# Kernel optimization log

Hardware: AMD Instinct MI355X
Metric: run time of the kernel (lower is better)

## Reference

```python
import jax, jax.numpy as jnp
import numpy as np

B, N = 16, 512          # graphs, nodes per graph (equal-size dynamic batch)
IN, HID, OUT, K = 256, 128, 256, 16  # hidden = in_dim // red_factor
EPS = 1e-5


def setup_inputs() -> dict:
    key = jax.random.key(0)
    ks = jax.random.split(key, 12)
    def lin(k, fi, fo):
        return jax.random.normal(k, (fi, fo), jnp.float32) / np.sqrt(fi).astype(np.float32)
    return {
        "obj_encs": jax.random.normal(ks[0], (B * N, IN), jnp.float32),
        "n_nodes": jnp.full((B,), N, dtype=jnp.int32),
        # self-graph-attention params (in -> hidden), with residual projection
        "Wq": lin(ks[1], IN, HID), "bq": jnp.zeros((HID,), jnp.float32),
        "Wk": lin(ks[2], IN, HID), "bk": jnp.zeros((HID,), jnp.float32),
        "Wv": lin(ks[3], IN, HID), "bv": jnp.zeros((HID,), jnp.float32),
        "Wr": lin(ks[4], IN, HID), "br": jnp.zeros((HID,), jnp.float32),
        # EdgeConv (local+global => 2*HID input features)
        "Wc": lin(ks[5], 2 * HID, OUT), "bc": jnp.zeros((OUT,), jnp.float32),
        # LayerNorm affine
        "ln_scale": jnp.ones((OUT,), jnp.float32),
        "ln_bias": jnp.zeros((OUT,), jnp.float32),
    }


def _forward(obj_encs, n_nodes, Wq, bq, Wk, bk, Wv, bv, Wr, br, Wc, bc, ln_scale, ln_bias):
    # dynamic batching: equal-size graphs per n_nodes -> reshape [B, N, IN]
    x = obj_encs.reshape(B, N, IN)

    # --- SelfGraphAttentionLinear (per-graph dot-product attention, residual) ---
    q = x @ Wq + bq                      # [B, N, HID]
    kk = x @ Wk + bk
    v = x @ Wv + bv
    attn = jax.nn.softmax(jnp.einsum('bnd,bmd->bnm', q, kk) / np.sqrt(HID).astype(np.float32), axis=-1)
    h = jnp.einsum('bnm,bmd->bnd', attn, v) + (x @ Wr + br)  # residual projection

    # --- GraphConv: kNN (euclidean) within each graph ---
    sq = jnp.sum(h * h, axis=-1)                             # [B, N]
    dist = sq[:, :, None] + sq[:, None, :] - 2.0 * jnp.einsum('bnd,bmd->bnm', h, h)
    _, idx = jax.lax.top_k(-dist, K)                         # [B, N, K] (self included)

    nb = jax.vmap(lambda hb, ib: hb[ib])(h, idx)             # [B, N, K, HID]
    hc = h[:, :, None, :]                                    # [B, N, 1, HID]
    # features='local+global': [x_i, x_j - x_i]
    e = jnp.concatenate([jnp.broadcast_to(hc, nb.shape), nb - hc], axis=-1)  # [B,N,K,2H]

    y = jnp.einsum('bnkf,fo->bnko', e, Wc) + bc              # [B, N, K, OUT]
    y = jnp.max(y, axis=2)                                   # reduction='max' over k

    mu = jnp.mean(y, axis=-1, keepdims=True)
    var = jnp.mean((y - mu) ** 2, axis=-1, keepdims=True)
    y = (y - mu) / jnp.sqrt(var + EPS) * ln_scale + ln_bias  # LayerNorm
    return jax.nn.selu(y).reshape(B * N, OUT)


def reference(obj_encs, n_nodes, Wq, bq, Wk, bk, Wv, bv, Wr, br, Wc, bc, ln_scale, ln_bias):
    return _forward(obj_encs, n_nodes, Wq, bq, Wk, bk, Wv, bv, Wr, br, Wc, bc, ln_scale, ln_bias)
```

## Files before the change

kernel.cpp:

```cpp
#include <hip/hip_runtime.h>
#include <math.h>

#define NB   16
#define NN   512
#define FIN  256
#define HID  128
#define FOUT 256
#define TOPK 16
#define ROWS (NB*NN)
#define LN_EPS 1e-5f

#define BK  32
#define LDK 40

typedef __attribute__((ext_vector_type(8))) short  bf16x8;
typedef __attribute__((ext_vector_type(4))) float  f32x4;

__device__ __forceinline__ ushort f2bf_rn(float x) {
    uint u = __float_as_uint(x);
    u += 0x7fff + ((u >> 16) & 1);
    return (ushort)(u >> 16);
}
__device__ __forceinline__ float bf2f(ushort h) {
    return __uint_as_float(((uint)h) << 16);
}
__device__ __forceinline__ void split2(float x, ushort& hi, ushort& lo) {
    hi = f2bf_rn(x);
    lo = f2bf_rn(x - bf2f(hi));
}

__device__ __forceinline__ void stage_rows64(ushort (*Dh)[LDK], ushort (*Dl)[LDK],
                                             const float* __restrict__ src,
                                             int rstride, int tid)
{
    const int r = tid >> 2, seg = (tid & 3) * 8;
    const float* p = src + (size_t)r * rstride + seg;
    #pragma unroll
    for (int i = 0; i < 2; i++) {
        const float4 q = *(const float4*)(p + 4*i);
        ushort h0,l0,h1,l1,h2,l2,h3,l3;
        split2(q.x,h0,l0); split2(q.y,h1,l1);
        split2(q.z,h2,l2); split2(q.w,h3,l3);
        *(ushort4*)&Dh[r][seg + 4*i] = make_ushort4(h0,h1,h2,h3);
        *(ushort4*)&Dl[r][seg + 4*i] = make_ushort4(l0,l1,l2,l3);
    }
}

__device__ __forceinline__ void stage_cols64(ushort (*Dh)[LDK], ushort (*Dl)[LDK],
                                             const float* __restrict__ src,
                                             int ldn, int tid)
{
    const int n = tid & 63, kh = (tid >> 6) * 8;
    const float* p = src + (size_t)kh * ldn + n;
    ushort hh[8], ll[8];
    #pragma unroll
    for (int i = 0; i < 8; i++) split2(p[(size_t)i * ldn], hh[i], ll[i]);
    *(ushort4*)&Dh[n][kh]     = make_ushort4(hh[0],hh[1],hh[2],hh[3]);
    *(ushort4*)&Dh[n][kh + 4] = make_ushort4(hh[4],hh[5],hh[6],hh[7]);
    *(ushort4*)&Dl[n][kh]     = make_ushort4(ll[0],ll[1],ll[2],ll[3]);
    *(ushort4*)&Dl[n][kh + 4] = make_ushort4(ll[4],ll[5],ll[6],ll[7]);
}

__device__ __forceinline__ void mma_step64(const ushort (*Ah)[LDK], const ushort (*Al)[LDK],
                                           const ushort (*Bh)[LDK], const ushort (*Bl)[LDK],
                                           f32x4 acc[2][2], int wr, int wc, int lane)
{
    const int q8 = (lane >> 4) * 8, m = lane & 15;
    bf16x8 ah[2], al[2], bh[2], bl[2];
    #pragma unroll
    for (int i = 0; i < 2; i++) {
        ah[i] = *(const bf16x8*)&Ah[wr + 16*i + m][q8];
        al[i] = *(const bf16x8*)&Al[wr + 16*i + m][q8];
        bh[i] = *(const bf16x8*)&Bh[wc + 16*i + m][q8];
        bl[i] = *(const bf16x8*)&Bl[wc + 16*i + m][q8];
    }
    #pragma unroll
    for (int i = 0; i < 2; i++)
        #pragma unroll
        for (int j = 0; j < 2; j++) {
            acc[i][j] = __builtin_amdgcn_mfma_f32_16x16x32_bf16(ah[i], bh[j], acc[i][j], 0, 0, 0);
            acc[i][j] = __builtin_amdgcn_mfma_f32_16x16x32_bf16(ah[i], bl[j], acc[i][j], 0, 0, 0);
            acc[i][j] = __builtin_amdgcn_mfma_f32_16x16x32_bf16(al[i], bh[j], acc[i][j], 0, 0, 0);
        }
}

#define MM64_PROLOGUE()                                                     \
    __shared__ ushort Ah[64][LDK], Al[64][LDK], Bh[64][LDK], Bl[64][LDK];   \
    const int tid = threadIdx.x, lane = tid & 63, wv = tid >> 6;            \
    const int wr = (wv >> 1) * 32, wc = (wv & 1) * 32;                      \
    f32x4 acc[2][2];                                                        \
    _Pragma("unroll")                                                       \
    for (int i = 0; i < 2; i++)                                             \
        _Pragma("unroll")                                                   \
        for (int j = 0; j < 2; j++)                                         \
            acc[i][j] = (f32x4){0.f, 0.f, 0.f, 0.f};

__global__ __launch_bounds__(256) void k_proj_m(
    const float* __restrict__ X,
    const float* __restrict__ Wq, const float* __restrict__ bq,
    const float* __restrict__ Wk, const float* __restrict__ bk,
    const float* __restrict__ Wv, const float* __restrict__ bv,
    const float* __restrict__ Wr, const float* __restrict__ br,
    float* __restrict__ Y)
{
    const int widx = blockIdx.x >> 1;
    const int ch   = (blockIdx.x & 1) * 64;
    const int br0  = blockIdx.y * 64;
    const float* W; const float* bias;
    if      (widx == 0) { W = Wq; bias = bq; }
    else if (widx == 1) { W = Wk; bias = bk; }
    else if (widx == 2) { W = Wv; bias = bv; }
    else                { W = Wr; bias = br; }

    MM64_PROLOGUE();

    for (int k0 = 0; k0 < FIN; k0 += BK) {
        stage_rows64(Ah, Al, X + (size_t)br0 * FIN + k0, FIN, tid);
        stage_cols64(Bh, Bl, W + (size_t)k0 * HID + ch, HID, tid);
        __syncthreads();
        mma_step64(Ah, Al, Bh, Bl, acc, wr, wc, lane);
        __syncthreads();
    }

    const int m = lane & 15, q4 = (lane >> 4) * 4;
    #pragma unroll
    for (int i = 0; i < 2; i++)
        #pragma unroll
        for (int reg = 0; reg < 4; reg++) {
            const int grow = br0 + wr + 16*i + q4 + reg;
            #pragma unroll
            for (int j = 0; j < 2; j++) {
                const int c = ch + wc + 16*j + m;
                Y[(size_t)grow * 512 + widx * 128 + c] = acc[i][j][reg] + bias[c];
            }
        }
}

__global__ __launch_bounds__(256) void k_scores_m(
    const float* __restrict__ Y, float* __restrict__ S)
{
    const int b = blockIdx.z;
    const int m0 = blockIdx.x * 64, n0 = blockIdx.y * 64;
    const float scale = 0.08838834764831845f;
    const float* Yb = Y + (size_t)b * NN * 512;

    MM64_PROLOGUE();

    for (int k0 = 0; k0 < HID; k0 += BK) {
        stage_rows64(Ah, Al, Yb + (size_t)n0 * 512 + k0,       512, tid);
        stage_rows64(Bh, Bl, Yb + (size_t)m0 * 512 + 128 + k0, 512, tid);
        __syncthreads();
        mma_step64(Ah, Al, Bh, Bl, acc, wr, wc, lane);
        __syncthreads();
    }

    float* Sb = S + (size_t)b * NN * NN;
    const int m = lane & 15, q4 = (lane >> 4) * 4;
    #pragma unroll
    for (int i = 0; i < 2; i++)
        #pragma unroll
        for (int reg = 0; reg < 4; reg++) {
            const int n = n0 + wr + 16*i + q4 + reg;
            #pragma unroll
            for (int j = 0; j < 2; j++)
                Sb[(size_t)n * NN + m0 + wc + 16*j + m] = acc[i][j][reg] * scale;
        }
}

__global__ __launch_bounds__(256) void k_softmax(float* __restrict__ S)
{
    float* p = S + (size_t)blockIdx.x * NN;
    const int tid = threadIdx.x;
    const int lane = tid & 63, wave = tid >> 6;
    __shared__ float red[4];

    float v0 = p[tid], v1 = p[tid + 256];
    float mx = fmaxf(v0, v1);
    #pragma unroll
    for (int off = 32; off > 0; off >>= 1) mx = fmaxf(mx, __shfl_down(mx, off));
    if (lane == 0) red[wave] = mx;
    __syncthreads();
    mx = fmaxf(fmaxf(red[0], red[1]), fmaxf(red[2], red[3]));
    __syncthreads();

    float e0 = __expf(v0 - mx), e1 = __expf(v1 - mx);
    float s = e0 + e1;
    #pragma unroll
    for (int off = 32; off > 0; off >>= 1) s += __shfl_down(s, off);
    if (lane == 0) red[wave] = s;
    __syncthreads();
    s = red[0] + red[1] + red[2] + red[3];
    const float inv = 1.0f / s;
    p[tid] = e0 * inv;
    p[tid + 256] = e1 * inv;
}

__global__ __launch_bounds__(256) void k_hgemm_m(
    const float* __restrict__ S, const float* __restrict__ Y,
    float* __restrict__ H)
{
    const int c0 = blockIdx.x * 64;
    const int n0 = blockIdx.y * 64;
    const int b  = blockIdx.z;
    const float* P = S + (size_t)b * NN * NN;

    MM64_PROLOGUE();

    for (int k0 = 0; k0 < NN; k0 += BK) {
        stage_rows64(Ah, Al, P + (size_t)n0 * NN + k0, NN, tid);
        stage_cols64(Bh, Bl, Y + ((size_t)(b * NN + k0)) * 512 + 256 + c0, 512, tid);
        __syncthreads();
        mma_step64(Ah, Al, Bh, Bl, acc, wr, wc, lane);
        __syncthreads();
    }

    const int m = lane & 15, q4 = (lane >> 4) * 4;
    #pragma unroll
    for (int i = 0; i < 2; i++)
        #pragma unroll
        for (int reg = 0; reg < 4; reg++) {
            const int gr = b * NN + n0 + wr + 16*i + q4 + reg;
            #pragma unroll
            for (int j = 0; j < 2; j++) {
                const int c = c0 + wc + 16*j + m;
                H[(size_t)gr * HID + c] = acc[i][j][reg] + Y[(size_t)gr * 512 + 384 + c];
            }
        }
}

__global__ __launch_bounds__(256) void k_sq(
    const float* __restrict__ H, float* __restrict__ SQ)
{
    const int row = blockIdx.x * 4 + (threadIdx.x >> 6);
    const int lane = threadIdx.x & 63;
    float a = H[(size_t)row*HID + lane];
    float c = H[(size_t)row*HID + 64 + lane];
    float s = a*a + c*c;
    #pragma unroll
    for (int off = 32; off > 0; off >>= 1) s += __shfl_down(s, off);
    if (lane == 0) SQ[row] = s;
}

__global__ __launch_bounds__(256) void k_ab_m(
    const float* __restrict__ H, const float* __restrict__ Wc,
    const float* __restrict__ bc, float* __restrict__ AB)
{
    const int ct  = blockIdx.x;
    const int br0 = blockIdx.y * 64;
    const bool bhalf = ct >= 4;
    const int c0 = (ct & 3) * 64;

    MM64_PROLOGUE();

    for (int k0 = 0; k0 < HID; k0 += BK) {
        stage_rows64(Ah, Al, H + (size_t)br0 * HID + k0, HID, tid);
        {
            const int n = tid & 63, kh = (tid >> 6) * 8;
            ushort hh[8], ll[8];
            #pragma unroll
            for (int i = 0; i < 8; i++) {
                const int k = k0 + kh + i;
                const float wbot = Wc[(size_t)(HID + k) * FOUT + c0 + n];
                const float val = bhalf ? wbot
                                        : (Wc[(size_t)k * FOUT + c0 + n] - wbot);
                split2(val, hh[i], ll[i]);
            }
            *(ushort4*)&Bh[n][kh]     = make_ushort4(hh[0],hh[1],hh[2],hh[3]);
            *(ushort4*)&Bh[n][kh + 4] = make_ushort4(hh[4],hh[5],hh[6],hh[7]);
            *(ushort4*)&Bl[n][kh]     = make_ushort4(ll[0],ll[1],ll[2],ll[3]);
            *(ushort4*)&Bl[n][kh + 4] = make_ushort4(ll[4],ll[5],ll[6],ll[7]);
        }
        __syncthreads();
        mma_step64(Ah, Al, Bh, Bl, acc, wr, wc, lane);
        __syncthreads();
    }

    const int m = lane & 15, q4 = (lane >> 4) * 4;
    #pragma unroll
    for (int i = 0; i < 2; i++)
        #pragma unroll
        for (int reg = 0; reg < 4; reg++) {
            const int grow = br0 + wr + 16*i + q4 + reg;
            #pragma unroll
            for (int j = 0; j < 2; j++) {
                const int c = wc + 16*j + m;
                const float add = bhalf ? 0.0f : bc[c0 + c];
                AB[(size_t)grow * 512 + ct * 64 + c] = acc[i][j][reg] + add;
            }
        }
}

__global__ __launch_bounds__(256) void k_dist_m(
    const float* __restrict__ H, const float* __restrict__ SQ,
    float* __restrict__ D)
{
    const int b = blockIdx.z;
    const int m0 = blockIdx.x * 64, n0 = blockIdx.y * 64;
    const float* Hb = H + (size_t)b * NN * HID;

    MM64_PROLOGUE();

    for (int k0 = 0; k0 < HID; k0 += BK) {
        stage_rows64(Ah, Al, Hb + (size_t)n0 * HID + k0, HID, tid);
        stage_rows64(Bh, Bl, Hb + (size_t)m0 * HID + k0, HID, tid);
        __syncthreads();
        mma_step64(Ah, Al, Bh, Bl, acc, wr, wc, lane);
        __syncthreads();
    }

    const int gb = b * NN;
    float* Db = D + (size_t)b * NN * NN;
    const int m = lane & 15, q4 = (lane >> 4) * 4;
    float sqm[2];
    #pragma unroll
    for (int j = 0; j < 2; j++) sqm[j] = SQ[gb + m0 + wc + 16*j + m];
    #pragma unroll
    for (int i = 0; i < 2; i++)
        #pragma unroll
        for (int reg = 0; reg < 4; reg++) {
            const int n = n0 + wr + 16*i + q4 + reg;
            const float sqn = SQ[gb + n];
            #pragma unroll
            for (int j = 0; j < 2; j++)
                Db[(size_t)n * NN + m0 + wc + 16*j + m]
                    = sqn + sqm[j] - 2.0f * acc[i][j][reg];
        }
}

__global__ __launch_bounds__(256) void k_out(
    const float* __restrict__ D, const float* __restrict__ AB,
    const float* __restrict__ ln_scale, const float* __restrict__ ln_bias,
    float* __restrict__ out)
{
    const int row  = blockIdx.x * 4 + (threadIdx.x >> 6);
    const int lane = threadIdx.x & 63;
    const int gb0  = row & ~(NN - 1);

    const float* drow = D + (size_t)row * NN;
    const float4 q0 = ((const float4*)drow)[lane];
    const float4 q1 = ((const float4*)drow)[64 + lane];
    float v[8] = {q0.x, q0.y, q0.z, q0.w, q1.x, q1.y, q1.z, q1.w};

    const float lsc0 = ln_scale[lane],       lbi0 = ln_bias[lane];
    const float lsc1 = ln_scale[lane + 64],  lbi1 = ln_bias[lane + 64];
    const float lsc2 = ln_scale[lane + 128], lbi2 = ln_bias[lane + 128];
    const float lsc3 = ln_scale[lane + 192], lbi3 = ln_bias[lane + 192];
    const float* arow = AB + (size_t)row * 512;
    const float a0 = arow[lane], a1 = arow[lane + 64],
                a2 = arow[lane + 128], a3 = arow[lane + 192];

    float bm0 = -INFINITY, bm1 = -INFINITY, bm2 = -INFINITY, bm3 = -INFINITY;

    for (int it = 0; it < TOPK; it++) {
        float bestv = v[0]; int bestm = 4*lane;
        #pragma unroll
        for (int j = 1; j < 8; j++) {
            const int m = (j >> 2)*256 + 4*lane + (j & 3);
            if (v[j] < bestv) { bestv = v[j]; bestm = m; }
        }
        #pragma unroll
        for (int off = 1; off < 64; off <<= 1) {
            const float ov = __shfl_xor(bestv, off);
            const int   om = __shfl_xor(bestm, off);
            if (ov < bestv || (ov == bestv && om < bestm)) { bestv = ov; bestm = om; }
        }
        const float* brow = AB + (size_t)(gb0 + bestm) * 512 + 256;
        bm0 = fmaxf(bm0, brow[lane]);
        bm1 = fmaxf(bm1, brow[lane + 64]);
        bm2 = fmaxf(bm2, brow[lane + 128]);
        bm3 = fmaxf(bm3, brow[lane + 192]);
        if (((bestm >> 2) & 63) == lane) {
            const int jj = ((bestm >> 8) << 2) | (bestm & 3);
            #pragma unroll
            for (int j = 0; j < 8; j++) if (j == jj) v[j] = INFINITY;
        }
    }

    float y0 = a0 + bm0, y1 = a1 + bm1, y2 = a2 + bm2, y3 = a3 + bm3;

    float s = y0 + y1 + y2 + y3;
    #pragma unroll
    for (int off = 1; off < 64; off <<= 1) s += __shfl_xor(s, off);
    const float mu = s * (1.0f/256.0f);
    const float d0 = y0 - mu, d1 = y1 - mu, d2 = y2 - mu, d3 = y3 - mu;
    float s2 = d0*d0 + d1*d1 + d2*d2 + d3*d3;
    #pragma unroll
    for (int off = 1; off < 64; off <<= 1) s2 += __shfl_xor(s2, off);
    const float var = s2 * (1.0f/256.0f);
    const float rstd = rsqrtf(var + LN_EPS);

    const float lam = 1.0507009873554805f, alpha = 1.6732632423543772f;
    float* orow = out + (size_t)row * FOUT;
    { const float z = d0*rstd*lsc0 + lbi0; orow[lane]       = z > 0.f ? lam*z : lam*alpha*expm1f(z); }
    { const float z = d1*rstd*lsc1 + lbi1; orow[lane + 64]  = z > 0.f ? lam*z : lam*alpha*expm1f(z); }
    { const float z = d2*rstd*lsc2 + lbi2; orow[lane + 128] = z > 0.f ? lam*z : lam*alpha*expm1f(z); }
    { const float z = d3*rstd*lsc3 + lbi3; orow[lane + 192] = z > 0.f ? lam*z : lam*alpha*expm1f(z); }
}

extern "C" void kernel_launch(void* const* d_in, const int* in_sizes, int n_in,
                              void* d_out, int out_size, void* d_ws, size_t ws_size,
                              hipStream_t stream)
{
    (void)in_sizes; (void)n_in; (void)out_size; (void)ws_size;
    const float* X   = (const float*)d_in[0];
    const float* Wq  = (const float*)d_in[2];
    const float* bq  = (const float*)d_in[3];
    const float* Wk  = (const float*)d_in[4];
    const float* bk  = (const float*)d_in[5];
    const float* Wv  = (const float*)d_in[6];
    const float* bv  = (const float*)d_in[7];
    const float* Wr  = (const float*)d_in[8];
    const float* br  = (const float*)d_in[9];
    const float* Wc  = (const float*)d_in[10];
    const float* bc  = (const float*)d_in[11];
    const float* lns = (const float*)d_in[12];
    const float* lnb = (const float*)d_in[13];
    float* out = (float*)d_out;

    float* ws = (float*)d_ws;
    float* Y  = ws;
    float* S  = Y + (size_t)ROWS*512;
    float* H  = S + (size_t)NB*NN*NN;
    float* SQ = H + (size_t)ROWS*HID;
    float* AB = SQ + ROWS;
    float* D  = S;

    k_proj_m  <<<dim3(8,128),  256, 0, stream>>>(X, Wq,bq, Wk,bk, Wv,bv, Wr,br, Y);
    k_scores_m<<<dim3(8,8,16), 256, 0, stream>>>(Y, S);
    k_softmax <<<ROWS,         256, 0, stream>>>(S);
    k_hgemm_m <<<dim3(2,8,16), 256, 0, stream>>>(S, Y, H);
    k_sq      <<<ROWS/4,       256, 0, stream>>>(H, SQ);
    k_ab_m    <<<dim3(8,128),  256, 0, stream>>>(H, Wc, bc, AB);
    k_dist_m  <<<dim3(8,8,16), 256, 0, stream>>>(H, SQ, D);
    k_out     <<<ROWS/4,       256, 0, stream>>>(D, AB, lns, lnb, out);
}
```

Measured before the change: 198.2 us.

## Pre-split operands to bf16 hi/lo in transposed layouts before GEMMs

Operands are now converted to bf16 hi/lo pairs once, in dedicated prep kernels or in producer epilogues, instead of being split inside every GEMM's shared-memory staging loop. Weights and V are stored transposed so all staging becomes plain vectorized 16-byte copies. The squared-norm kernel is folded into the attention-output GEMM epilogue using atomics. This removes repeated split arithmetic and strided column loads, at the cost of two extra launches and more workspace traffic.

```diff
diff --git a/kernel.cpp b/kernel.cpp
--- a/kernel.cpp
+++ b/kernel.cpp
@@ -13,8 +13,9 @@
 #define BK  32
 #define LDK 40
 
-typedef __attribute__((ext_vector_type(8))) short  bf16x8;
-typedef __attribute__((ext_vector_type(4))) float  f32x4;
+typedef __attribute__((ext_vector_type(8)))  short  bf16x8;
+typedef __attribute__((ext_vector_type(4)))  float  f32x4;
+typedef __attribute__((ext_vector_type(8)))  unsigned short u16x8;
 
 __device__ __forceinline__ ushort f2bf_rn(float x) {
     uint u = __float_as_uint(x);
@@ -29,36 +30,11 @@
     lo = f2bf_rn(x - bf2f(hi));
 }
 
-__device__ __forceinline__ void stage_rows64(ushort (*Dh)[LDK], ushort (*Dl)[LDK],
-                                             const float* __restrict__ src,
-                                             int rstride, int tid)
+__device__ __forceinline__ void stage_u(ushort (*Ds)[LDK], const ushort* __restrict__ src,
+                                        int rstride, int tid)
 {
     const int r = tid >> 2, seg = (tid & 3) * 8;
-    const float* p = src + (size_t)r * rstride + seg;
-    #pragma unroll
-    for (int i = 0; i < 2; i++) {
-        const float4 q = *(const float4*)(p + 4*i);
-        ushort h0,l0,h1,l1,h2,l2,h3,l3;
-        split2(q.x,h0,l0); split2(q.y,h1,l1);
-        split2(q.z,h2,l2); split2(q.w,h3,l3);
-        *(ushort4*)&Dh[r][seg + 4*i] = make_ushort4(h0,h1,h2,h3);
-        *(ushort4*)&Dl[r][seg + 4*i] = make_ushort4(l0,l1,l2,l3);
-    }
-}
-
-__device__ __forceinline__ void stage_cols64(ushort (*Dh)[LDK], ushort (*Dl)[LDK],
-                                             const float* __restrict__ src,
-                                             int ldn, int tid)
-{
-    const int n = tid & 63, kh = (tid >> 6) * 8;
-    const float* p = src + (size_t)kh * ldn + n;
-    ushort hh[8], ll[8];
-    #pragma unroll
-    for (int i = 0; i < 8; i++) split2(p[(size_t)i * ldn], hh[i], ll[i]);
-    *(ushort4*)&Dh[n][kh]     = make_ushort4(hh[0],hh[1],hh[2],hh[3]);
-    *(ushort4*)&Dh[n][kh + 4] = make_ushort4(hh[4],hh[5],hh[6],hh[7]);
-    *(ushort4*)&Dl[n][kh]     = make_ushort4(ll[0],ll[1],ll[2],ll[3]);
-    *(ushort4*)&Dl[n][kh + 4] = make_ushort4(ll[4],ll[5],ll[6],ll[7]);
+    *(u16x8*)&Ds[r][seg] = *(const u16x8*)(src + (size_t)r * rstride + seg);
 }
 
 __device__ __forceinline__ void mma_step64(const ushort (*Ah)[LDK], const ushort (*Al)[LDK],
@@ -85,7 +61,12 @@
 }
 
 #define MM64_PROLOGUE()                                                     \
-    __shared__ ushort Ah[64][LDK], Al[64][LDK], Bh[64][LDK], Bl[64][LDK];   \
+    __shared__ ushort smem[4*64*LDK];                                       \
+    ushort (*Ah)[LDK] = (ushort (*)[LDK])(smem);                            \
+    ushort (*Al)[LDK] = (ushort (*)[LDK])(smem + 64*LDK);                   \
+    ushort (*Bh)[LDK] = (ushort (*)[LDK])(smem + 2*64*LDK);                 \
+    ushort (*Bl)[LDK] = (ushort (*)[LDK])(smem + 3*64*LDK);                 \
+    float* fbuf = (float*)smem;   \
     const int tid = threadIdx.x, lane = tid & 63, wv = tid >> 6;            \
     const int wr = (wv >> 1) * 32, wc = (wv & 1) * 32;                      \
     f32x4 acc[2][2];                                                        \
@@ -95,60 +76,208 @@
         for (int j = 0; j < 2; j++)                                         \
             acc[i][j] = (f32x4){0.f, 0.f, 0.f, 0.f};
 
+__global__ __launch_bounds__(256) void k_prep_w(
+    const float* __restrict__ Wq, const float* __restrict__ Wk,
+    const float* __restrict__ Wv, const float* __restrict__ Wr,
+    const float* __restrict__ Wc,
+    const float* __restrict__ bq, const float* __restrict__ bk,
+    const float* __restrict__ bv, const float* __restrict__ br,
+    const float* __restrict__ bc,
+    ushort* __restrict__ Wth, ushort* __restrict__ Wtl,
+    ushort* __restrict__ Wcth, ushort* __restrict__ Wctl,
+    float* __restrict__ bcat, float* __restrict__ bcab,
+    float* __restrict__ SQ)
+{
+    const int blk = blockIdx.x, tid = threadIdx.x;
+    __shared__ float fb[64][65];
+
+    if (blk < 8) {
+        const int n0 = blk * 64;
+        const int widx = n0 >> 7;
+        const float* W = widx==0 ? Wq : widx==1 ? Wk : widx==2 ? Wv : Wr;
+        const int cbase = n0 & 127;
+        for (int kt = 0; kt < 4; kt++) {
+            const int k0 = kt * 64;
+            __syncthreads();
+            {
+                const int kk = tid >> 2, cs = (tid & 3) * 16;
+                #pragma unroll
+                for (int t = 0; t < 16; t += 4) {
+                    const float4 q = *(const float4*)&W[(size_t)(k0+kk)*HID + cbase + cs + t];
+                    fb[kk][cs+t]=q.x; fb[kk][cs+t+1]=q.y; fb[kk][cs+t+2]=q.z; fb[kk][cs+t+3]=q.w;
+                }
+            }
+            __syncthreads();
+            {
+                const int c = tid >> 2, ks = (tid & 3) * 16;
+                u16x8 vh0, vh1, vl0, vl1;
+                #pragma unroll
+                for (int t = 0; t < 8; t++) {
+                    ushort hh, ll;
+                    split2(fb[ks+t][c], hh, ll); vh0[t]=hh; vl0[t]=ll;
+                    split2(fb[ks+8+t][c], hh, ll); vh1[t]=hh; vl1[t]=ll;
+                }
+                *(u16x8*)&Wth[(size_t)(n0+c)*256 + k0 + ks]     = vh0;
+                *(u16x8*)&Wth[(size_t)(n0+c)*256 + k0 + ks + 8] = vh1;
+                *(u16x8*)&Wtl[(size_t)(n0+c)*256 + k0 + ks]     = vl0;
+                *(u16x8*)&Wtl[(size_t)(n0+c)*256 + k0 + ks + 8] = vl1;
+            }
+        }
+    } else if (blk < 16) {
+        const int n0 = (blk - 8) * 64;
+        const bool ahalf = n0 < 256;
+        const int cbase = n0 & 255;
+        for (int kt = 0; kt < 2; kt++) {
+            const int k0 = kt * 64;
+            __syncthreads();
+            {
+                const int kk = tid >> 2, cs = (tid & 3) * 16;
+                #pragma unroll
+                for (int t = 0; t < 16; t++) {
+                    const float bot = Wc[(size_t)(HID + k0 + kk)*FOUT + cbase + cs + t];
+                    float val = bot;
+                    if (ahalf) val = Wc[(size_t)(k0 + kk)*FOUT + cbase + cs + t] - bot;
+                    fb[kk][cs+t] = val;
+                }
+            }
+            __syncthreads();
+            {
+                const int c = tid >> 2, ks = (tid & 3) * 16;
+                u16x8 vh0, vh1, vl0, vl1;
+                #pragma unroll
+                for (int t = 0; t < 8; t++) {
+                    ushort hh, ll;
+                    split2(fb[ks+t][c], hh, ll); vh0[t]=hh; vl0[t]=ll;
+                    split2(fb[ks+8+t][c], hh, ll); vh1[t]=hh; vl1[t]=ll;
+                }
+                *(u16x8*)&Wcth[(size_t)(n0+c)*128 + k0 + ks]     = vh0;
+                *(u16x8*)&Wcth[(size_t)(n0+c)*128 + k0 + ks + 8] = vh1;
+                *(u16x8*)&Wctl[(size_t)(n0+c)*128 + k0 + ks]     = vl0;
+                *(u16x8*)&Wctl[(size_t)(n0+c)*128 + k0 + ks + 8] = vl1;
+            }
+        }
+    } else {
+        for (int i = tid; i < 512; i += 256) {
+            const int w = i >> 7, c = i & 127;
+            bcat[i] = w==0 ? bq[c] : w==1 ? bk[c] : w==2 ? bv[c] : br[c];
+            bcab[i] = i < 256 ? bc[i] : 0.f;
+        }
+        for (int i = tid; i < ROWS; i += 256) SQ[i] = 0.f;
+    }
+}
+
+__global__ __launch_bounds__(256) void k_prep_x(
+    const float* __restrict__ X, ushort* __restrict__ Xh, ushort* __restrict__ Xl)
+{
+    const size_t base = ((size_t)blockIdx.x * 256 + threadIdx.x) * 8;
+    const float4 a = *(const float4*)(X + base);
+    const float4 b = *(const float4*)(X + base + 4);
+    u16x8 vh, vl; ushort hh, ll;
+    split2(a.x,hh,ll); vh[0]=hh; vl[0]=ll;
+    split2(a.y,hh,ll); vh[1]=hh; vl[1]=ll;
+    split2(a.z,hh,ll); vh[2]=hh; vl[2]=ll;
+    split2(a.w,hh,ll); vh[3]=hh; vl[3]=ll;
+    split2(b.x,hh,ll); vh[4]=hh; vl[4]=ll;
+    split2(b.y,hh,ll); vh[5]=hh; vl[5]=ll;
+    split2(b.z,hh,ll); vh[6]=hh; vl[6]=ll;
+    split2(b.w,hh,ll); vh[7]=hh; vl[7]=ll;
+    *(u16x8*)(Xh + base) = vh;
+    *(u16x8*)(Xl + base) = vl;
+}
+
 __global__ __launch_bounds__(256) void k_proj_m(
-    const float* __restrict__ X,
-    const float* __restrict__ Wq, const float* __restrict__ bq,
-    const float* __restrict__ Wk, const float* __restrict__ bk,
-    const float* __restrict__ Wv, const float* __restrict__ bv,
-    const float* __restrict__ Wr, const float* __restrict__ br,
-    float* __restrict__ Y)
-{
-    const int widx = blockIdx.x >> 1;
-    const int ch   = (blockIdx.x & 1) * 64;
-    const int br0  = blockIdx.y * 64;
-    const float* W; const float* bias;
-    if      (widx == 0) { W = Wq; bias = bq; }
-    else if (widx == 1) { W = Wk; bias = bk; }
-    else if (widx == 2) { W = Wv; bias = bv; }
-    else                { W = Wr; bias = br; }
+    const ushort* __restrict__ Xh, const ushort* __restrict__ Xl,
+    const ushort* __restrict__ Wth, const ushort* __restrict__ Wtl,
+    const float* __restrict__ bcat,
+    ushort* __restrict__ Yh, ushort* __restrict__ Yl,
+    ushort* __restrict__ Vth, ushort* __restrict__ Vtl,
+    float* __restrict__ Rbuf)
+{
+    const int ct  = blockIdx.x;
+    const int br0 = blockIdx.y * 64;
 
     MM64_PROLOGUE();
 
     for (int k0 = 0; k0 < FIN; k0 += BK) {
-        stage_rows64(Ah, Al, X + (size_t)br0 * FIN + k0, FIN, tid);
-        stage_cols64(Bh, Bl, W + (size_t)k0 * HID + ch, HID, tid);
+        stage_u(Ah, Xh + (size_t)br0 * 256 + k0, 256, tid);
+        stage_u(Al, Xl + (size_t)br0 * 256 + k0, 256, tid);
+        stage_u(Bh, Wth + (size_t)(ct*64) * 256 + k0, 256, tid);
+        stage_u(Bl, Wtl + (size_t)(ct*64) * 256 + k0, 256, tid);
         __syncthreads();
         mma_step64(Ah, Al, Bh, Bl, acc, wr, wc, lane);
         __syncthreads();
     }
 
-    const int m = lane & 15, q4 = (lane >> 4) * 4;
-    #pragma unroll
-    for (int i = 0; i < 2; i++)
-        #pragma unroll
-        for (int reg = 0; reg < 4; reg++) {
-            const int grow = br0 + wr + 16*i + q4 + reg;
+    {
+        const int m = lane & 15, q4 = (lane >> 4) * 4;
+        #pragma unroll
+        for (int i = 0; i < 2; i++)
             #pragma unroll
-            for (int j = 0; j < 2; j++) {
-                const int c = ch + wc + 16*j + m;
-                Y[(size_t)grow * 512 + widx * 128 + c] = acc[i][j][reg] + bias[c];
-            }
-        }
+            for (int reg = 0; reg < 4; reg++) {
+                const int r = wr + 16*i + q4 + reg;
+                #pragma unroll
+                for (int j = 0; j < 2; j++) {
+                    const int c = wc + 16*j + m;
+                    fbuf[r*65 + c] = acc[i][j][reg] + bcat[ct*64 + c];
+                }
+            }
+    }
+    __syncthreads();
+
+    if (ct < 4) {
+        const int r = tid >> 2, cs = (tid & 3) * 16;
+        u16x8 vh0, vh1, vl0, vl1;
+        #pragma unroll
+        for (int t = 0; t < 8; t++) {
+            ushort hh, ll;
+            split2(fbuf[r*65 + cs + t], hh, ll);     vh0[t]=hh; vl0[t]=ll;
+            split2(fbuf[r*65 + cs + 8 + t], hh, ll); vh1[t]=hh; vl1[t]=ll;
+        }
+        const size_t o = (size_t)(br0 + r) * 256 + ct*64 + cs;
+        *(u16x8*)&Yh[o]   = vh0; *(u16x8*)&Yh[o+8] = vh1;
+        *(u16x8*)&Yl[o]   = vl0; *(u16x8*)&Yl[o+8] = vl1;
+    } else if (ct < 6) {
+        const int cl = tid >> 2, rs = (tid & 3) * 16;
+        const int b = br0 >> 9, nb = br0 & 511;
+        const int cglob = (ct - 4) * 64 + cl;
+        u16x8 vh0, vh1, vl0, vl1;
+        #pragma unroll
+        for (int t = 0; t < 8; t++) {
+            ushort hh, ll;
+            split2(fbuf[(rs+t)*65 + cl], hh, ll);   vh0[t]=hh; vl0[t]=ll;
+            split2(fbuf[(rs+8+t)*65 + cl], hh, ll); vh1[t]=hh; vl1[t]=ll;
+        }
+        const size_t o = ((size_t)b*128 + cglob) * 512 + nb + rs;
+        *(u16x8*)&Vth[o]   = vh0; *(u16x8*)&Vth[o+8] = vh1;
+        *(u16x8*)&Vtl[o]   = vl0; *(u16x8*)&Vtl[o+8] = vl1;
+    } else {
+        const int r = tid >> 2, cs = (tid & 3) * 16;
+        float* dst = Rbuf + (size_t)(br0 + r) * 128 + (ct - 6)*64 + cs;
+        #pragma unroll
+        for (int t = 0; t < 16; t += 4) {
+            float4 q;
+            q.x = fbuf[r*65+cs+t];   q.y = fbuf[r*65+cs+t+1];
+            q.z = fbuf[r*65+cs+t+2]; q.w = fbuf[r*65+cs+t+3];
+            *(float4*)(dst + t) = q;
+        }
+    }
 }
 
 __global__ __launch_bounds__(256) void k_scores_m(
-    const float* __restrict__ Y, float* __restrict__ S)
+    const ushort* __restrict__ Yh, const ushort* __restrict__ Yl,
+    float* __restrict__ S)
 {
     const int b = blockIdx.z;
     const int m0 = blockIdx.x * 64, n0 = blockIdx.y * 64;
     const float scale = 0.08838834764831845f;
-    const float* Yb = Y + (size_t)b * NN * 512;
 
     MM64_PROLOGUE();
 
     for (int k0 = 0; k0 < HID; k0 += BK) {
-        stage_rows64(Ah, Al, Yb + (size_t)n0 * 512 + k0,       512, tid);
-        stage_rows64(Bh, Bl, Yb + (size_t)m0 * 512 + 128 + k0, 512, tid);
+        stage_u(Ah, Yh + (size_t)(b*NN + n0) * 256 + k0,       256, tid);
+        stage_u(Al, Yl + (size_t)(b*NN + n0) * 256 + k0,       256, tid);
+        stage_u(Bh, Yh + (size_t)(b*NN + m0) * 256 + 128 + k0, 256, tid);
+        stage_u(Bl, Yl + (size_t)(b*NN + m0) * 256 + 128 + k0, 256, tid);
         __syncthreads();
         mma_step64(Ah, Al, Bh, Bl, acc, wr, wc, lane);
         __syncthreads();
@@ -167,15 +296,16 @@
         }
 }
 
-__global__ __launch_bounds__(256) void k_softmax(float* __restrict__ S)
-{
-    float* p = S + (size_t)blockIdx.x * NN;
-    const int tid = threadIdx.x;
-    const int lane = tid & 63, wave = tid >> 6;
+__global__ __launch_bounds__(256) void k_softmax2(
+    const float* __restrict__ S, ushort* __restrict__ Ph, ushort* __restrict__ Pl)
+{
+    const size_t row = blockIdx.x;
+    const float* p = S + row * NN;
+    const int tid = threadIdx.x, lane = tid & 63, wave = tid >> 6;
     __shared__ float red[4];
 
-    float v0 = p[tid], v1 = p[tid + 256];
-    float mx = fmaxf(v0, v1);
+    const float2 vv = ((const float2*)p)[tid];
+    float mx = fmaxf(vv.x, vv.y);
     #pragma unroll
     for (int off = 32; off > 0; off >>= 1) mx = fmaxf(mx, __shfl_down(mx, off));
     if (lane == 0) red[wave] = mx;
@@ -183,7 +313,7 @@
     mx = fmaxf(fmaxf(red[0], red[1]), fmaxf(red[2], red[3]));
     __syncthreads();
 
-    float e0 = __expf(v0 - mx), e1 = __expf(v1 - mx);
+    const float e0 = __expf(vv.x - mx), e1 = __expf(vv.y - mx);
     float s = e0 + e1;
     #pragma unroll
     for (int off = 32; off > 0; off >>= 1) s += __shfl_down(s, off);
@@ -191,85 +321,96 @@
     __syncthreads();
     s = red[0] + red[1] + red[2] + red[3];
     const float inv = 1.0f / s;
-    p[tid] = e0 * inv;
-    p[tid + 256] = e1 * inv;
+
+    ushort h0,l0,h1,l1;
+    split2(e0 * inv, h0, l0);
+    split2(e1 * inv, h1, l1);
+    ((ushort2*)Ph)[row * 256 + tid] = make_ushort2(h0, h1);
+    ((ushort2*)Pl)[row * 256 + tid] = make_ushort2(l0, l1);
 }
 
 __global__ __launch_bounds__(256) void k_hgemm_m(
-    const float* __restrict__ S, const float* __restrict__ Y,
-    float* __restrict__ H)
+    const ushort* __restrict__ Ph, const ushort* __restrict__ Pl,
+    const ushort* __restrict__ Vth, const ushort* __restrict__ Vtl,
+    const float* __restrict__ Rbuf,
+    ushort* __restrict__ Hh, ushort* __restrict__ Hl,
+    float* __restrict__ SQ)
 {
     const int c0 = blockIdx.x * 64;
     const int n0 = blockIdx.y * 64;
     const int b  = blockIdx.z;
-    const float* P = S + (size_t)b * NN * NN;
 
     MM64_PROLOGUE();
 
     for (int k0 = 0; k0 < NN; k0 += BK) {
-        stage_rows64(Ah, Al, P + (size_t)n0 * NN + k0, NN, tid);
-        stage_cols64(Bh, Bl, Y + ((size_t)(b * NN + k0)) * 512 + 256 + c0, 512, tid);
+        stage_u(Ah, Ph + (size_t)(b*NN + n0) * 512 + k0, 512, tid);
+        stage_u(Al, Pl + (size_t)(b*NN + n0) * 512 + k0, 512, tid);
+        stage_u(Bh, Vth + ((size_t)b*128 + c0) * 512 + k0, 512, tid);
+        stage_u(Bl, Vtl + ((size_t)b*128 + c0) * 512 + k0, 512, tid);
         __syncthreads();
         mma_step64(Ah, Al, Bh, Bl, acc, wr, wc, lane);
         __syncthreads();
     }
 
-    const int m = lane & 15, q4 = (lane >> 4) * 4;
-    #pragma unroll
-    for (int i = 0; i < 2; i++)
-        #pragma unroll
-        for (int reg = 0; reg < 4; reg++) {
-            const int gr = b * NN + n0 + wr + 16*i + q4 + reg;
+    {
+        const int m = lane & 15, q4 = (lane >> 4) * 4;
+        #pragma unroll
+        for (int i = 0; i < 2; i++)
             #pragma unroll
-            for (int j = 0; j < 2; j++) {
-                const int c = c0 + wc + 16*j + m;
-                H[(size_t)gr * HID + c] = acc[i][j][reg] + Y[(size_t)gr * 512 + 384 + c];
-            }
-        }
-}
-
-__global__ __launch_bounds__(256) void k_sq(
-    const float* __restrict__ H, float* __restrict__ SQ)
-{
-    const int row = blockIdx.x * 4 + (threadIdx.x >> 6);
-    const int lane = threadIdx.x & 63;
-    float a = H[(size_t)row*HID + lane];
-    float c = H[(size_t)row*HID + 64 + lane];
-    float s = a*a + c*c;
-    #pragma unroll
-    for (int off = 32; off > 0; off >>= 1) s += __shfl_down(s, off);
-    if (lane == 0) SQ[row] = s;
+            for (int reg = 0; reg < 4; reg++) {
+                const int r = wr + 16*i + q4 + reg;
+                #pragma unroll
+                for (int j = 0; j < 2; j++)
+                    fbuf[r*65 + wc + 16*j + m] = acc[i][j][reg];
+            }
+    }
+    __syncthreads();
+
+    {
+        const int r = tid >> 2, cs = (tid & 3) * 16;
+        const int gr = b*NN + n0 + r;
+        const float* rp = Rbuf + (size_t)gr * 128 + c0 + cs;
+        float h[16]; float sqp = 0.f;
+        #pragma unroll
+        for (int t = 0; t < 16; t += 4) {
+            const float4 q = *(const float4*)(rp + t);
+            h[t]   = fbuf[r*65+cs+t]   + q.x;
+            h[t+1] = fbuf[r*65+cs+t+1] + q.y;
+            h[t+2] = fbuf[r*65+cs+t+2] + q.z;
+            h[t+3] = fbuf[r*65+cs+t+3] + q.w;
+        }
+        u16x8 vh0, vh1, vl0, vl1;
+        #pragma unroll
+        for (int t = 0; t < 8; t++) {
+            ushort hh, ll;
+            split2(h[t], hh, ll);   vh0[t]=hh; vl0[t]=ll;
+            split2(h[8+t], hh, ll); vh1[t]=hh; vl1[t]=ll;
+            sqp += h[t]*h[t] + h[8+t]*h[8+t];
+        }
+        const size_t o = (size_t)gr * 128 + c0 + cs;
+        *(u16x8*)&Hh[o]   = vh0; *(u16x8*)&Hh[o+8] = vh1;
+        *(u16x8*)&Hl[o]   = vl0; *(u16x8*)&Hl[o+8] = vl1;
+        sqp += __shfl_xor(sqp, 1);
+        sqp += __shfl_xor(sqp, 2);
+        if ((tid & 3) == 0) atomicAdd(&SQ[gr], sqp);
+    }
 }
 
 __global__ __launch_bounds__(256) void k_ab_m(
-    const float* __restrict__ H, const float* __restrict__ Wc,
-    const float* __restrict__ bc, float* __restrict__ AB)
+    const ushort* __restrict__ Hh, const ushort* __restrict__ Hl,
+    const ushort* __restrict__ Wcth, const ushort* __restrict__ Wctl,
+    const float* __restrict__ bcab, float* __restrict__ AB)
 {
     const int ct  = blockIdx.x;
     const int br0 = blockIdx.y * 64;
-    const bool bhalf = ct >= 4;
-    const int c0 = (ct & 3) * 64;
 
     MM64_PROLOGUE();
 
     for (int k0 = 0; k0 < HID; k0 += BK) {
-        stage_rows64(Ah, Al, H + (size_t)br0 * HID + k0, HID, tid);
-        {
-            const int n = tid & 63, kh = (tid >> 6) * 8;
-            ushort hh[8], ll[8];
-            #pragma unroll
-            for (int i = 0; i < 8; i++) {
-                const int k = k0 + kh + i;
-                const float wbot = Wc[(size_t)(HID + k) * FOUT + c0 + n];
-                const float val = bhalf ? wbot
-                                        : (Wc[(size_t)k * FOUT + c0 + n] - wbot);
-                split2(val, hh[i], ll[i]);
-            }
-            *(ushort4*)&Bh[n][kh]     = make_ushort4(hh[0],hh[1],hh[2],hh[3]);
-            *(ushort4*)&Bh[n][kh + 4] = make_ushort4(hh[4],hh[5],hh[6],hh[7]);
-            *(ushort4*)&Bl[n][kh]     = make_ushort4(ll[0],ll[1],ll[2],ll[3]);
-            *(ushort4*)&Bl[n][kh + 4] = make_ushort4(ll[4],ll[5],ll[6],ll[7]);
-        }
+        stage_u(Ah, Hh + (size_t)br0 * 128 + k0, 128, tid);
+        stage_u(Al, Hl + (size_t)br0 * 128 + k0, 128, tid);
+        stage_u(Bh, Wcth + (size_t)(ct*64) * 128 + k0, 128, tid);
+        stage_u(Bl, Wctl + (size_t)(ct*64) * 128 + k0, 128, tid);
         __syncthreads();
         mma_step64(Ah, Al, Bh, Bl, acc, wr, wc, lane);
         __syncthreads();
@@ -284,25 +425,25 @@
             #pragma unroll
             for (int j = 0; j < 2; j++) {
                 const int c = wc + 16*j + m;
-                const float add = bhalf ? 0.0f : bc[c0 + c];
-                AB[(size_t)grow * 512 + ct * 64 + c] = acc[i][j][reg] + add;
+                AB[(size_t)grow * 512 + ct*64 + c] = acc[i][j][reg] + bcab[ct*64 + c];
             }
         }
 }
 
 __global__ __launch_bounds__(256) void k_dist_m(
-    const float* __restrict__ H, const float* __restrict__ SQ,
-    float* __restrict__ D)
+    const ushort* __restrict__ Hh, const ushort* __restrict__ Hl,
+    const float* __restrict__ SQ, float* __restrict__ D)
 {
     const int b = blockIdx.z;
     const int m0 = blockIdx.x * 64, n0 = blockIdx.y * 64;
-    const float* Hb = H + (size_t)b * NN * HID;
 
     MM64_PROLOGUE();
 
     for (int k0 = 0; k0 < HID; k0 += BK) {
-        stage_rows64(Ah, Al, Hb + (size_t)n0 * HID + k0, HID, tid);
-        stage_rows64(Bh, Bl, Hb + (size_t)m0 * HID + k0, HID, tid);
+        stage_u(Ah, Hh + (size_t)(b*NN + n0) * 128 + k0, 128, tid);
+        stage_u(Al, Hl + (size_t)(b*NN + n0) * 128 + k0, 128, tid);
+        stage_u(Bh, Hh + (size_t)(b*NN + m0) * 128 + k0, 128, tid);
+        stage_u(Bl, Hl + (size_t)(b*NN + m0) * 128 + k0, 128, tid);
         __syncthreads();
         mma_step64(Ah, Al, Bh, Bl, acc, wr, wc, lane);
         __syncthreads();
@@ -417,20 +558,39 @@
     const float* lnb = (const float*)d_in[13];
     float* out = (float*)d_out;
 
-    float* ws = (float*)d_ws;
-    float* Y  = ws;
-    float* S  = Y + (size_t)ROWS*512;
-    float* H  = S + (size_t)NB*NN*NN;
-    float* SQ = H + (size_t)ROWS*HID;
-    float* AB = SQ + ROWS;
-    float* D  = S;
-
-    k_proj_m  <<<dim3(8,128),  256, 0, stream>>>(X, Wq,bq, Wk,bk, Wv,bv, Wr,br, Y);
-    k_scores_m<<<dim3(8,8,16), 256, 0, stream>>>(Y, S);
-    k_softmax <<<ROWS,         256, 0, stream>>>(S);
-    k_hgemm_m <<<dim3(2,8,16), 256, 0, stream>>>(S, Y, H);
-    k_sq      <<<ROWS/4,       256, 0, stream>>>(H, SQ);
-    k_ab_m    <<<dim3(8,128),  256, 0, stream>>>(H, Wc, bc, AB);
-    k_dist_m  <<<dim3(8,8,16), 256, 0, stream>>>(H, SQ, D);
+    char* cur = (char*)d_ws;
+    auto alloc = [&](size_t bytes) { char* p = cur; cur += (bytes + 255) & ~size_t(255); return p; };
+
+    float*  S    = (float*)alloc((size_t)NB*NN*NN*4);
+    float*  AB   = (float*)alloc((size_t)ROWS*512*4);
+    float*  Rbuf = (float*)alloc((size_t)ROWS*128*4);
+    float*  SQ   = (float*)alloc((size_t)ROWS*4);
+    float*  bcat = (float*)alloc(512*4);
+    float*  bcab = (float*)alloc(512*4);
+    ushort* Xh   = (ushort*)alloc((size_t)ROWS*256*2);
+    ushort* Xl   = (ushort*)alloc((size_t)ROWS*256*2);
+    ushort* Yh   = (ushort*)alloc((size_t)ROWS*256*2);
+    ushort* Yl   = (ushort*)alloc((size_t)ROWS*256*2);
+    ushort* Vth  = (ushort*)alloc((size_t)NB*128*512*2);
+    ushort* Vtl  = (ushort*)alloc((size_t)NB*128*512*2);
+    ushort* Ph   = (ushort*)alloc((size_t)ROWS*512*2);
+    ushort* Pl   = (ushort*)alloc((size_t)ROWS*512*2);
+    ushort* Hh   = (ushort*)alloc((size_t)ROWS*128*2);
+    ushort* Hl   = (ushort*)alloc((size_t)ROWS*128*2);
+    ushort* Wth  = (ushort*)alloc((size_t)512*256*2);
+    ushort* Wtl  = (ushort*)alloc((size_t)512*256*2);
+    ushort* Wcth = (ushort*)alloc((size_t)512*128*2);
+    ushort* Wctl = (ushort*)alloc((size_t)512*128*2);
+    float*  D    = S;
+
+    k_prep_w  <<<17,           256, 0, stream>>>(Wq,Wk,Wv,Wr,Wc, bq,bk,bv,br,bc,
+                                                 Wth,Wtl,Wcth,Wctl, bcat,bcab, SQ);
+    k_prep_x  <<<ROWS*256/(256*8), 256, 0, stream>>>(X, Xh, Xl);
+    k_proj_m  <<<dim3(8,128),  256, 0, stream>>>(Xh,Xl, Wth,Wtl, bcat, Yh,Yl, Vth,Vtl, Rbuf);
+    k_scores_m<<<dim3(8,8,16), 256, 0, stream>>>(Yh,Yl, S);
+    k_softmax2<<<ROWS,         256, 0, stream>>>(S, Ph, Pl);
+    k_hgemm_m <<<dim3(2,8,16), 256, 0, stream>>>(Ph,Pl, Vth,Vtl, Rbuf, Hh,Hl, SQ);
+    k_ab_m    <<<dim3(8,128),  256, 0, stream>>>(Hh,Hl, Wcth,Wctl, bcab, AB);
+    k_dist_m  <<<dim3(8,8,16), 256, 0, stream>>>(Hh,Hl, SQ, D);
     k_out     <<<ROWS/4,       256, 0, stream>>>(D, AB, lns, lnb, out);
 }
```

Result: no change. 196.5 us (-0.9%).
